# Kernel tuning notes

Hardware: AMD Instinct MI355X
Metric: run time of the kernel (lower is better)

The kernel has to match this reference:

```python
import jax, jax.numpy as jnp
import numpy as np

HID, PROJ, ATTN = 512, 1024, 128
B, L = 4, 2048


def _apply_rope(x):
    # x: [B, L, 2, ATTN]; RoPE over sequence dim (axis=1)
    half = x.shape[-1] // 2
    inv_freq = jnp.power(10000.0, -jnp.arange(half, dtype=jnp.float32) / half)
    pos = jnp.arange(x.shape[1], dtype=x.dtype)
    sinusoid = pos[:, None] * inv_freq.astype(x.dtype)          # [L, half]
    sin = jnp.sin(sinusoid)[None, :, None, :]                   # [1, L, 1, half]
    cos = jnp.cos(sinusoid)[None, :, None, :]
    x1, x2 = jnp.split(x, 2, axis=-1)
    return jnp.concatenate([x1 * cos - x2 * sin, x2 * cos + x1 * sin], axis=-1)


def setup_inputs() -> dict:
    key = jax.random.key(0)
    ks = jax.random.split(key, 8)
    node = jax.random.normal(ks[0], (B, L, HID), dtype=jnp.float32)
    bias = jax.random.normal(ks[1], (B, L, L), dtype=jnp.float32)
    scaling = jnp.full((1,), ATTN ** -0.5, dtype=jnp.float32)
    w1 = jax.random.normal(ks[2], (HID, 2 * PROJ + ATTN), dtype=jnp.float32) * (HID ** -0.5)
    b1 = jnp.zeros((2 * PROJ + ATTN,), dtype=jnp.float32)
    ms_weight = jax.random.normal(ks[3], (2, ATTN), dtype=jnp.float32) * 0.02
    ms_bias = jnp.zeros((2, ATTN), dtype=jnp.float32)
    w2 = jax.random.normal(ks[4], (PROJ, HID), dtype=jnp.float32) * (PROJ ** -0.5)
    b2 = jnp.zeros((HID,), dtype=jnp.float32)
    return {"node": node, "bias": bias, "scaling": scaling, "w1": w1, "b1": b1,
            "ms_weight": ms_weight, "ms_bias": ms_bias, "w2": w2, "b2": b2}


def reference(node, bias, scaling, w1, b1, ms_weight, ms_bias, w2, b2):
    # gated projection + SiLU
    gva = jax.nn.silu(node @ w1 + b1)                           # [B, L, 2P+A]
    gates, values, base = jnp.split(gva, [PROJ, 2 * PROJ], axis=-1)
    # multi-headed scaling -> [B, L, 2, A], then RoPE, then split q/k
    qk = base[..., None, :] * ms_weight + ms_bias               # [B, L, 2, A]
    qk = _apply_rope(qk)
    q, k = qk[..., 0, :], qk[..., 1, :]                         # [B, L, A]
    logits = jnp.einsum('bid,bjd->bij', q * scaling, k) + bias  # [B, L, L]
    attn = jax.nn.softmax(logits, axis=-1)
    out = jnp.einsum('bij,bjd->bid', attn, values)              # [B, L, P]
    return (out * gates) @ w2 + b2                              # [B, L, HID]
```

## Files before the change

kernel.cpp:

```cpp
#include <hip/hip_runtime.h>
#include <math.h>

#define HIDN 512
#define PROJ 1024
#define ATTN 128
#define BATCH 4
#define SEQ 2048
#define N1 (2*PROJ+ATTN)
#define ROWS (BATCH*SEQ)
#define QR 16

typedef __attribute__((ext_vector_type(4))) float f32x4;
typedef __attribute__((ext_vector_type(8))) short bf16x8;

__device__ __forceinline__ short f2bf(float x){
    unsigned u = __builtin_bit_cast(unsigned, x);
    unsigned rounding = 0x7fffu + ((u >> 16) & 1u);
    u += rounding;
    return (short)(u >> 16);
}
__device__ __forceinline__ float bf2f(short s){
    unsigned u = ((unsigned)(unsigned short)s) << 16;
    return __builtin_bit_cast(float, u);
}

__device__ __forceinline__ void gload16(const void* g, void* l){
    __builtin_amdgcn_global_load_lds((const __attribute__((address_space(1))) void*)g,
                                     (__attribute__((address_space(3))) void*)l,
                                     16, 0, 0);
}

template<int BK, class Epi>
__device__ __forceinline__ void gemm_bt_tile(const short* __restrict__ A, int lda,
                                             const short* __restrict__ BT, int ldb,
                                             int m0, int n0, int K, Epi epi)
{
    __shared__ __align__(16) short lA[2][128*BK];
    __shared__ __align__(16) short lB[2][128*BK];
    const int t = threadIdx.x;
    const int lane = t & 63;
    const int w = t >> 6;
    const int wr = (w >> 1) * 64, wc = (w & 1) * 64;
    const int half = lane >> 4, l16 = lane & 15;
    constexpr int SPT = BK/16;

    f32x4 acc[4][4];
    #pragma unroll
    for (int i=0;i<4;i++)
        #pragma unroll
        for (int j=0;j<4;j++)
            acc[i][j] = (f32x4){0.f,0.f,0.f,0.f};

    auto stage = [&](int buf, int k0){
        #pragma unroll
        for (int i = 0; i < SPT; i++) {
            int li = i*256 + t;
            int r = li / (BK/8), s = li % (BK/8);
            int ss = (BK==64) ? (s ^ (r & 7)) : (s ^ ((r >> 1) & 3));
            gload16(A + (size_t)(m0+r)*lda + k0 + ss*8, lA[buf] + li*8);
        }
        #pragma unroll
        for (int i = 0; i < SPT; i++) {
            int li = i*256 + t;
            int r = li / (BK/8), s = li % (BK/8);
            int ss = (BK==64) ? (s ^ (r & 7)) : (s ^ ((r >> 1) & 3));
            gload16(BT + (size_t)(n0+r)*ldb + k0 + ss*8, lB[buf] + li*8);
        }
    };

    stage(0, 0);
    __syncthreads();
    int cur = 0;
    for (int k0 = BK; k0 <= K; k0 += BK) {
        if (k0 < K) stage(cur^1, k0);
        #pragma unroll
        for (int kk = 0; kk < BK; kk += 32) {
            bf16x8 af[4], bfr[4];
            const int cs = (kk >> 3) + half;
            #pragma unroll
            for (int i=0;i<4;i++){
                int row = wr + i*16 + l16;
                int sl = (BK==64) ? (cs ^ (row & 7)) : (cs ^ ((row >> 1) & 3));
                af[i] = *(const bf16x8*)(lA[cur] + row*BK + sl*8);
            }
            #pragma unroll
            for (int j=0;j<4;j++){
                int row = wc + j*16 + l16;
                int sl = (BK==64) ? (cs ^ (row & 7)) : (cs ^ ((row >> 1) & 3));
                bfr[j] = *(const bf16x8*)(lB[cur] + row*BK + sl*8);
            }
            #pragma unroll
            for (int i=0;i<4;i++)
                #pragma unroll
                for (int j=0;j<4;j++)
                    acc[i][j] = __builtin_amdgcn_mfma_f32_16x16x32_bf16(af[i], bfr[j], acc[i][j], 0, 0, 0);
        }
        __syncthreads();
        cur ^= 1;
    }
    #pragma unroll
    for (int i=0;i<4;i++)
        #pragma unroll
        for (int j=0;j<4;j++)
            #pragma unroll
            for (int q=0;q<4;q++)
                epi(m0 + wr + i*16 + half*4 + q, n0 + wc + j*16 + l16, acc[i][j][q]);
}

__global__ void k_cast_node(const float* __restrict__ in, short* __restrict__ out){
    int idx = blockIdx.x*256 + threadIdx.x;
    const float4 v = ((const float4*)in)[idx];
    short4 o; o.x = f2bf(v.x); o.y = f2bf(v.y); o.z = f2bf(v.z); o.w = f2bf(v.w);
    ((short4*)out)[idx] = o;
}

__global__ void k_transpose_cast(const float* __restrict__ in, short* __restrict__ out,
                                 int R, int C){
    __shared__ short tile[64][65];
    int r0 = blockIdx.y*64, c0 = blockIdx.x*64;
    int t = threadIdx.x;
    #pragma unroll
    for (int i=0;i<16;i++){
        int lin = i*256 + t; int r = lin>>6, c = lin&63;
        tile[r][c] = f2bf(in[(size_t)(r0+r)*C + c0+c]);
    }
    __syncthreads();
    #pragma unroll
    for (int i=0;i<16;i++){
        int lin = i*256 + t; int c = lin>>6, r = lin&63;
        out[(size_t)(c0+c)*R + r0+r] = tile[r][c];
    }
}

__global__ void k_transpose_v(const short* __restrict__ values, short* __restrict__ VT){
    __shared__ short tile[64][65];
    int z = blockIdx.z;
    int c0 = blockIdx.x*64, r0 = blockIdx.y*64;
    int t = threadIdx.x;
    #pragma unroll
    for (int i=0;i<16;i++){
        int lin = i*256 + t; int r = lin>>6, c = lin&63;
        tile[r][c] = values[(size_t)(z*SEQ + r0+r)*PROJ + c0+c];
    }
    __syncthreads();
    #pragma unroll
    for (int i=0;i<16;i++){
        int lin = i*256 + t; int c = lin>>6, r = lin&63;
        VT[((size_t)z*PROJ + c0+c)*SEQ + r0+r] = tile[r][c];
    }
}

__global__ __launch_bounds__(256) void k_mm1(const short* __restrict__ nodeb,
        const short* __restrict__ w1T, const float* __restrict__ b1,
        short* __restrict__ gates, short* __restrict__ values, short* __restrict__ baseb){
    int b = blockIdx.x;
    int wg = (b & 7) * (N1/128*64/8) + (b >> 3);
    int n0 = (wg % (N1/128))*128, m0 = (wg / (N1/128))*128;
    gemm_bt_tile<32>(nodeb, HIDN, w1T, HIDN, m0, n0, HIDN,
        [=](int row, int col, float v){
            v += b1[col];
            v = v / (1.f + __expf(-v));
            short bv = f2bf(v);
            if (col < PROJ)        gates [(size_t)row*PROJ + col]        = bv;
            else if (col < 2*PROJ) values[(size_t)row*PROJ + col-PROJ]   = bv;
            else                   baseb [(size_t)row*ATTN + col-2*PROJ] = bv;
        });
}

__global__ void k_rope2(const short* __restrict__ baseb, const float* __restrict__ msw,
                        const float* __restrict__ msb, const float* __restrict__ scaling,
                        short* __restrict__ qb, short* __restrict__ kb){
    int idx = blockIdx.x*256 + threadIdx.x;
    int d = idx & 63;
    int row = idx >> 6;
    int l = row & (SEQ-1);
    float inv = exp2f(-(float)d * (13.287712379549449f/64.f));
    float ang = (float)l * inv;
    float s = sinf(ang), c = cosf(ang);
    const short* bp = baseb + (size_t)row*ATTN;
    float b_lo = bf2f(bp[d]), b_hi = bf2f(bp[d+64]);
    float x1q = b_lo*msw[d]        + msb[d];
    float x2q = b_hi*msw[d+64]     + msb[d+64];
    float x1k = b_lo*msw[128+d]    + msb[128+d];
    float x2k = b_hi*msw[128+d+64] + msb[128+d+64];
    float sc = scaling[0];
    qb[(size_t)row*ATTN + d]    = f2bf((x1q*c - x2q*s)*sc);
    qb[(size_t)row*ATTN + d+64] = f2bf((x2q*c + x1q*s)*sc);
    kb[(size_t)row*ATTN + d]    = f2bf(x1k*c - x2k*s);
    kb[(size_t)row*ATTN + d+64] = f2bf(x2k*c + x1k*s);
}

__global__ __launch_bounds__(512, 4) void k_qksm(
        const short* __restrict__ qg, const short* __restrict__ kg,
        const float* __restrict__ bias, short* __restrict__ P,
        float* __restrict__ lsum)
{
    __shared__ short ptw[8][16][56];
    __shared__ float s_l[8][16];

    const int z = blockIdx.y;
    const int r0 = blockIdx.x * QR;
    const int kvh = blockIdx.z;
    const int kv0 = kvh * 1024;
    const int t = threadIdx.x;
    const int w = t >> 6;
    const int lane = t & 63;
    const int l16 = lane & 15, half = lane >> 4;

    const short* Q  = qg + ((size_t)z*SEQ + r0)*ATTN;
    const short* K  = kg + (size_t)z*SEQ*ATTN;
    const float* Bb = bias + ((size_t)z*SEQ + r0)*SEQ;
    short* Pp = P + ((size_t)z*SEQ + r0)*SEQ;

    bf16x8 qf[4];
    #pragma unroll
    for (int kc=0;kc<4;kc++)
        qf[kc] = *(const bf16x8*)(Q + (size_t)l16*ATTN + kc*32 + half*8);

    f32x4 ts = (f32x4){0.f,0.f,0.f,0.f};

    float bn[2][4];
    #pragma unroll
    for (int j=0;j<2;j++)
        #pragma unroll
        for (int e=0;e<4;e++)
            bn[j][e] = Bb[(size_t)(half*4+e)*SEQ + kv0 + w*32 + j*16 + l16];

    #pragma unroll 2
    for (int c=0; c<4; c++){
        float bx[2][4];
        if (c < 3){
            #pragma unroll
            for (int j=0;j<2;j++)
                #pragma unroll
                for (int e=0;e<4;e++)
                    bx[j][e] = Bb[(size_t)(half*4+e)*SEQ + kv0 + (c+1)*256 + w*32 + j*16 + l16];
        }
        #pragma unroll
        for (int j=0;j<2;j++){
            const int kvb = kv0 + c*256 + w*32 + j*16;
            const short* Kc = K + (size_t)(kvb + l16)*ATTN;
            f32x4 a = (f32x4){bn[j][0], bn[j][1], bn[j][2], bn[j][3]};
            #pragma unroll
            for (int kc=0;kc<4;kc++){
                bf16x8 kf = *(const bf16x8*)(Kc + kc*32 + half*8);
                a = __builtin_amdgcn_mfma_f32_16x16x32_bf16(qf[kc], kf, a, 0,0,0);
            }
            float p0 = __expf(a[0]), p1 = __expf(a[1]);
            float p2 = __expf(a[2]), p3 = __expf(a[3]);
            ts[0] += p0; ts[1] += p1; ts[2] += p2; ts[3] += p3;
            ptw[w][half*4+0][j*16+l16] = f2bf(p0);
            ptw[w][half*4+1][j*16+l16] = f2bf(p1);
            ptw[w][half*4+2][j*16+l16] = f2bf(p2);
            ptw[w][half*4+3][j*16+l16] = f2bf(p3);
        }
        {
            bf16x8 v = *(const bf16x8*)&ptw[w][lane>>2][(lane&3)*8];
            *(bf16x8*)(Pp + (size_t)(lane>>2)*SEQ + kv0 + c*256 + w*32 + (lane&3)*8) = v;
        }
        #pragma unroll
        for (int j=0;j<2;j++)
            #pragma unroll
            for (int e=0;e<4;e++)
                bn[j][e] = bx[j][e];
    }

    #pragma unroll
    for (int e=0;e<4;e++){
        ts[e] += __shfl_xor(ts[e],1,64);
        ts[e] += __shfl_xor(ts[e],2,64);
        ts[e] += __shfl_xor(ts[e],4,64);
        ts[e] += __shfl_xor(ts[e],8,64);
    }
    if (l16 == 0){
        #pragma unroll
        for (int e=0;e<4;e++) s_l[w][half*4+e] = ts[e];
    }
    __syncthreads();
    if (t < 16){
        float sum = 0.f;
        #pragma unroll
        for (int ww=0; ww<8; ww++) sum += s_l[ww][t];
        lsum[(size_t)kvh*ROWS + (size_t)z*SEQ + r0 + t] = sum;
    }
}

__global__ __launch_bounds__(256) void k_pv2(const short* __restrict__ P,
        const short* __restrict__ VT, const short* __restrict__ gates,
        const float* __restrict__ lsum, short* __restrict__ a2){
    int b = blockIdx.x;
    int wg = (b & 7) * 64 + (b >> 3);
    int xx = wg & 7, yy = (wg >> 3) & 15, z = wg >> 7;
    const short* A = P  + (size_t)z*SEQ*SEQ;
    const short* B = VT + (size_t)z*PROJ*SEQ;
    int n0 = xx*128, m0 = yy*128;
    gemm_bt_tile<64>(A, SEQ, B, SEQ, m0, n0, SEQ,
        [=](int r, int c, float v){
            size_t ri = (size_t)z*SEQ + r;
            float li = 1.f / (lsum[ri] + lsum[(size_t)ROWS + ri]);
            size_t gi = ri*PROJ + c;
            a2[gi] = f2bf(v * li * bf2f(gates[gi]));
        });
}

__global__ __launch_bounds__(256) void k_mm2(const short* __restrict__ a2,
        const short* __restrict__ w2T, const float* __restrict__ b2,
        float* __restrict__ out){
    int b = blockIdx.x;
    int wg = (b & 7) * 32 + (b >> 3);
    int n0 = (wg & 3)*128, m0 = (wg >> 2)*128;
    gemm_bt_tile<32>(a2, PROJ, w2T, PROJ, m0, n0, PROJ,
        [=](int r, int c, float v){
            out[(size_t)r*HIDN + c] = v + b2[c];
        });
}

extern "C" void kernel_launch(void* const* d_in, const int* in_sizes, int n_in,
                              void* d_out, int out_size, void* d_ws, size_t ws_size,
                              hipStream_t stream) {
    const float* node    = (const float*)d_in[0];
    const float* bias    = (const float*)d_in[1];
    const float* scaling = (const float*)d_in[2];
    const float* w1      = (const float*)d_in[3];
    const float* b1      = (const float*)d_in[4];
    const float* msw     = (const float*)d_in[5];
    const float* msb     = (const float*)d_in[6];
    const float* w2      = (const float*)d_in[7];
    const float* b2      = (const float*)d_in[8];
    float* out = (float*)d_out;

    char* p = (char*)d_ws;
    auto alloc = [&](size_t bytes){ char* r = p; p += (bytes + 255) & ~(size_t)255; return r; };
    short* nodeb  = (short*)alloc((size_t)ROWS*HIDN*2);
    short* w1T    = (short*)alloc((size_t)N1*HIDN*2);
    short* w2T    = (short*)alloc((size_t)HIDN*PROJ*2);
    short* gates  = (short*)alloc((size_t)ROWS*PROJ*2);
    short* values = (short*)alloc((size_t)ROWS*PROJ*2);
    short* VT     = (short*)alloc((size_t)BATCH*PROJ*SEQ*2);
    short* baseb  = (short*)alloc((size_t)ROWS*ATTN*2);
    short* qb     = (short*)alloc((size_t)ROWS*ATTN*2);
    short* kb     = (short*)alloc((size_t)ROWS*ATTN*2);
    short* Pbuf   = (short*)alloc((size_t)BATCH*SEQ*SEQ*2);
    float* lsum   = (float*)alloc((size_t)2*ROWS*4);
    short* a2buf  = (short*)alloc((size_t)ROWS*PROJ*2);

    k_cast_node<<<ROWS*HIDN/1024, 256, 0, stream>>>(node, nodeb);
    k_transpose_cast<<<dim3(N1/64, HIDN/64), 256, 0, stream>>>(w1, w1T, HIDN, N1);
    k_transpose_cast<<<dim3(HIDN/64, PROJ/64), 256, 0, stream>>>(w2, w2T, PROJ, HIDN);
    k_mm1<<<(N1/128)*(ROWS/128), 256, 0, stream>>>(nodeb, w1T, b1, gates, values, baseb);
    k_transpose_v<<<dim3(PROJ/64, SEQ/64, BATCH), 256, 0, stream>>>(values, VT);
    k_rope2<<<ROWS*64/256, 256, 0, stream>>>(baseb, msw, msb, scaling, qb, kb);
    k_qksm<<<dim3(SEQ/QR, BATCH, 2), 512, 0, stream>>>(qb, kb, bias, Pbuf, lsum);
    k_pv2<<<(PROJ/128)*(SEQ/128)*BATCH, 256, 0, stream>>>(Pbuf, VT, gates, lsum, a2buf);
    k_mm2<<<(HIDN/128)*(ROWS/128), 256, 0, stream>>>(a2buf, w2T, b2, out);
}
```

Before: 166.0 us.

## Write values transposed from mm1 epilogue; defer P stores in qksm

The mm1 epilogue now writes the SiLU'd value columns straight into the transposed VT layout, which removes the separate transpose kernel and the round trip through the intermediate values buffer. Separately, the QK softmax kernel now fully unrolls its chunk loop, keeps the bf16-packed probabilities in registers, and writes them to LDS and global memory after all MFMA work is done. The transposed epilogue store is strided across rows, so its global writes may coalesce poorly. Holding the probabilities in registers also raises register pressure in the attention kernel.

```diff
diff --git a/kernel.cpp b/kernel.cpp
--- a/kernel.cpp
+++ b/kernel.cpp
@@ -132,27 +132,9 @@
     }
 }
 
-__global__ void k_transpose_v(const short* __restrict__ values, short* __restrict__ VT){
-    __shared__ short tile[64][65];
-    int z = blockIdx.z;
-    int c0 = blockIdx.x*64, r0 = blockIdx.y*64;
-    int t = threadIdx.x;
-    #pragma unroll
-    for (int i=0;i<16;i++){
-        int lin = i*256 + t; int r = lin>>6, c = lin&63;
-        tile[r][c] = values[(size_t)(z*SEQ + r0+r)*PROJ + c0+c];
-    }
-    __syncthreads();
-    #pragma unroll
-    for (int i=0;i<16;i++){
-        int lin = i*256 + t; int c = lin>>6, r = lin&63;
-        VT[((size_t)z*PROJ + c0+c)*SEQ + r0+r] = tile[r][c];
-    }
-}
-
 __global__ __launch_bounds__(256) void k_mm1(const short* __restrict__ nodeb,
         const short* __restrict__ w1T, const float* __restrict__ b1,
-        short* __restrict__ gates, short* __restrict__ values, short* __restrict__ baseb){
+        short* __restrict__ gates, short* __restrict__ VT, short* __restrict__ baseb){
     int b = blockIdx.x;
     int wg = (b & 7) * (N1/128*64/8) + (b >> 3);
     int n0 = (wg % (N1/128))*128, m0 = (wg / (N1/128))*128;
@@ -161,8 +143,11 @@
             v += b1[col];
             v = v / (1.f + __expf(-v));
             short bv = f2bf(v);
-            if (col < PROJ)        gates [(size_t)row*PROJ + col]        = bv;
-            else if (col < 2*PROJ) values[(size_t)row*PROJ + col-PROJ]   = bv;
+            if (col < PROJ)        gates [(size_t)row*PROJ + col] = bv;
+            else if (col < 2*PROJ){
+                int z = row >> 11, r = row & (SEQ-1);
+                VT[((size_t)z*PROJ + (col-PROJ))*SEQ + r] = bv;
+            }
             else                   baseb [(size_t)row*ATTN + col-2*PROJ] = bv;
         });
 }
@@ -218,6 +203,7 @@
         qf[kc] = *(const bf16x8*)(Q + (size_t)l16*ATTN + kc*32 + half*8);
 
     f32x4 ts = (f32x4){0.f,0.f,0.f,0.f};
+    unsigned pk[4][4];
 
     float bn[2][4];
     #pragma unroll
@@ -226,7 +212,7 @@
         for (int e=0;e<4;e++)
             bn[j][e] = Bb[(size_t)(half*4+e)*SEQ + kv0 + w*32 + j*16 + l16];
 
-    #pragma unroll 2
+    #pragma unroll
     for (int c=0; c<4; c++){
         float bx[2][4];
         if (c < 3){
@@ -249,20 +235,28 @@
             float p0 = __expf(a[0]), p1 = __expf(a[1]);
             float p2 = __expf(a[2]), p3 = __expf(a[3]);
             ts[0] += p0; ts[1] += p1; ts[2] += p2; ts[3] += p3;
-            ptw[w][half*4+0][j*16+l16] = f2bf(p0);
-            ptw[w][half*4+1][j*16+l16] = f2bf(p1);
-            ptw[w][half*4+2][j*16+l16] = f2bf(p2);
-            ptw[w][half*4+3][j*16+l16] = f2bf(p3);
-        }
-        {
-            bf16x8 v = *(const bf16x8*)&ptw[w][lane>>2][(lane&3)*8];
-            *(bf16x8*)(Pp + (size_t)(lane>>2)*SEQ + kv0 + c*256 + w*32 + (lane&3)*8) = v;
+            pk[c][j*2+0] = (unsigned)(unsigned short)f2bf(p0) | ((unsigned)(unsigned short)f2bf(p1)<<16);
+            pk[c][j*2+1] = (unsigned)(unsigned short)f2bf(p2) | ((unsigned)(unsigned short)f2bf(p3)<<16);
         }
         #pragma unroll
         for (int j=0;j<2;j++)
             #pragma unroll
             for (int e=0;e<4;e++)
                 bn[j][e] = bx[j][e];
+    }
+
+    #pragma unroll
+    for (int c=0; c<4; c++){
+        #pragma unroll
+        for (int j=0;j<2;j++){
+            unsigned u0 = pk[c][j*2+0], u1 = pk[c][j*2+1];
+            ptw[w][half*4+0][j*16+l16] = (short)(u0 & 0xffff);
+            ptw[w][half*4+1][j*16+l16] = (short)(u0 >> 16);
+            ptw[w][half*4+2][j*16+l16] = (short)(u1 & 0xffff);
+            ptw[w][half*4+3][j*16+l16] = (short)(u1 >> 16);
+        }
+        bf16x8 v = *(const bf16x8*)&ptw[w][lane>>2][(lane&3)*8];
+        *(bf16x8*)(Pp + (size_t)(lane>>2)*SEQ + kv0 + c*256 + w*32 + (lane&3)*8) = v;
     }
 
     #pragma unroll
@@ -335,7 +329,6 @@
     short* w1T    = (short*)alloc((size_t)N1*HIDN*2);
     short* w2T    = (short*)alloc((size_t)HIDN*PROJ*2);
     short* gates  = (short*)alloc((size_t)ROWS*PROJ*2);
-    short* values = (short*)alloc((size_t)ROWS*PROJ*2);
     short* VT     = (short*)alloc((size_t)BATCH*PROJ*SEQ*2);
     short* baseb  = (short*)alloc((size_t)ROWS*ATTN*2);
     short* qb     = (short*)alloc((size_t)ROWS*ATTN*2);
@@ -347,8 +340,7 @@
     k_cast_node<<<ROWS*HIDN/1024, 256, 0, stream>>>(node, nodeb);
     k_transpose_cast<<<dim3(N1/64, HIDN/64), 256, 0, stream>>>(w1, w1T, HIDN, N1);
     k_transpose_cast<<<dim3(HIDN/64, PROJ/64), 256, 0, stream>>>(w2, w2T, PROJ, HIDN);
-    k_mm1<<<(N1/128)*(ROWS/128), 256, 0, stream>>>(nodeb, w1T, b1, gates, values, baseb);
-    k_transpose_v<<<dim3(PROJ/64, SEQ/64, BATCH), 256, 0, stream>>>(values, VT);
+    k_mm1<<<(N1/128)*(ROWS/128), 256, 0, stream>>>(nodeb, w1T, b1, gates, VT, baseb);
     k_rope2<<<ROWS*64/256, 256, 0, stream>>>(baseb, msw, msb, scaling, qb, kb);
     k_qksm<<<dim3(SEQ/QR, BATCH, 2), 512, 0, stream>>>(qb, kb, bias, Pbuf, lsum);
     k_pv2<<<(PROJ/128)*(SEQ/128)*BATCH, 256, 0, stream>>>(Pbuf, VT, gates, lsum, a2buf);
```

New measurement: 173.4 us. +4.4%, slower.
